# Optimization experiments

Measured on AMD Instinct MI355X. Metric: run time of the kernel, lower is better.

## Reference

```python
import jax, jax.numpy as jnp
import numpy as np

N, E, F_IN, HID, HEADS, B, CLASSES = 50000, 800000, 128, 64, 4, 512, 2


def setup_inputs() -> dict:
    key = jax.random.key(0)
    ks = jax.random.split(key, 20)
    s = 0.05
    inp = {
        "x": jax.random.normal(ks[0], (N, F_IN), jnp.float32),
        "edge_index": jax.random.randint(ks[1], (2, E), 0, N, jnp.int32),
        "batch": jnp.sort(jax.random.randint(ks[2], (N,), 0, B, jnp.int32)),
        # GCN layers (3): layer0 F_IN->HID, layers 1,2 HID->HID
        "gcn_w0": jax.random.normal(ks[3], (F_IN, HID), jnp.float32) * s,
        "gcn_b0": jnp.zeros((HID,), jnp.float32),
        "gcn_w1": jax.random.normal(ks[4], (HID, HID), jnp.float32) * s,
        "gcn_b1": jnp.zeros((HID,), jnp.float32),
        "gcn_w2": jax.random.normal(ks[5], (HID, HID), jnp.float32) * s,
        "gcn_b2": jnp.zeros((HID,), jnp.float32),
        # GAT: W [HID, HEADS*HID], attention vectors [HEADS, HID], bias [HID] (concat=False)
        "gat_w": jax.random.normal(ks[6], (HID, HEADS * HID), jnp.float32) * s,
        "gat_att_src": jax.random.normal(ks[7], (HEADS, HID), jnp.float32) * s,
        "gat_att_dst": jax.random.normal(ks[8], (HEADS, HID), jnp.float32) * s,
        "gat_b": jnp.zeros((HID,), jnp.float32),
        # MLP head
        "lin1_w": jax.random.normal(ks[9], (HID, HID // 2), jnp.float32) * s,
        "lin1_b": jnp.zeros((HID // 2,), jnp.float32),
        "lin2_w": jax.random.normal(ks[10], (HID // 2, CLASSES), jnp.float32) * s,
        "lin2_b": jnp.zeros((CLASSES,), jnp.float32),
    }
    return inp


def _forward(x, edge_index, batch,
             gcn_w0, gcn_b0, gcn_w1, gcn_b1, gcn_w2, gcn_b2,
             gat_w, gat_att_src, gat_att_dst, gat_b,
             lin1_w, lin1_b, lin2_w, lin2_b):
    n = x.shape[0]
    loop = jnp.arange(n, dtype=edge_index.dtype)
    src = jnp.concatenate([edge_index[0], loop])  # [E+N] with self-loops
    dst = jnp.concatenate([edge_index[1], loop])

    # symmetric GCN normalization (self-loops included, deg >= 1)
    deg = jax.ops.segment_sum(jnp.ones_like(dst, dtype=x.dtype), dst, num_segments=n)
    dinv = jax.lax.rsqrt(jnp.maximum(deg, 1.0))
    norm = dinv[src] * dinv[dst]  # [E+N]

    for W, b in ((gcn_w0, gcn_b0), (gcn_w1, gcn_b1), (gcn_w2, gcn_b2)):
        h = x @ W  # [N, HID]
        x = jax.ops.segment_sum(h[src] * norm[:, None], dst, num_segments=n) + b
        x = jax.nn.relu(x)  # dropout is identity in eval mode

    # GAT layer (heads=HEADS, concat=False -> mean over heads)
    H, C = gat_att_src.shape
    h = (x @ gat_w).reshape(n, H, C)  # [N, H, C]
    a_src = jnp.einsum('nhc,hc->nh', h, gat_att_src)
    a_dst = jnp.einsum('nhc,hc->nh', h, gat_att_dst)
    e = jax.nn.leaky_relu(a_src[src] + a_dst[dst], 0.2)  # [E+N, H]
    m = jax.ops.segment_max(e, dst, num_segments=n)      # per-dst softmax max
    p = jnp.exp(e - m[dst])
    denom = jax.ops.segment_sum(p, dst, num_segments=n)
    alpha = p / denom[dst]                                # [E+N, H]
    out = jax.ops.segment_sum(h[src] * alpha[:, :, None], dst, num_segments=n)
    x = jax.nn.relu(out.mean(axis=1) + gat_b)             # [N, HID]

    # global mean pool + global max pool over graphs
    cnt = jax.ops.segment_sum(jnp.ones((n,), x.dtype), batch, num_segments=B)
    mean_p = jax.ops.segment_sum(x, batch, num_segments=B) / jnp.maximum(cnt, 1.0)[:, None]
    max_p = jax.ops.segment_max(x, batch, num_segments=B)
    max_p = jnp.where(cnt[:, None] > 0, max_p, 0.0)
    g = mean_p + max_p  # [B, HID]

    g = jax.nn.relu(g @ lin1_w + lin1_b)
    return g @ lin2_w + lin2_b  # [B, CLASSES]


def reference(x, edge_index, batch,
              gcn_w0, gcn_b0, gcn_w1, gcn_b1, gcn_w2, gcn_b2,
              gat_w, gat_att_src, gat_att_dst, gat_b,
              lin1_w, lin1_b, lin2_w, lin2_b):
    return _forward(x, edge_index, batch,
                    gcn_w0, gcn_b0, gcn_w1, gcn_b1, gcn_w2, gcn_b2,
                    gat_w, gat_att_src, gat_att_dst, gat_b,
                    lin1_w, lin1_b, lin2_w, lin2_b)
```

## Files before the change

### kernel.cpp

```cpp
#include <hip/hip_runtime.h>
#include <math.h>

typedef short bf8 __attribute__((ext_vector_type(8)));
typedef _Float16 h8 __attribute__((ext_vector_type(8)));
typedef float f4 __attribute__((ext_vector_type(4)));
typedef unsigned short ushort_t;

#define BRANGE 128
#define NB_E 256

__device__ __forceinline__ int ilanebcast(int v, int l) {
  return __builtin_amdgcn_readlane(v, l);
}

__device__ __forceinline__ float wave_sum(float v) {
#pragma unroll
  for (int off = 32; off > 0; off >>= 1) v += __shfl_xor(v, off, 64);
  return v;
}

__device__ __forceinline__ ushort_t f2bf(float x) {
  unsigned int u = __float_as_uint(x);
  return (ushort_t)((u + 0x7fffu + ((u >> 16) & 1u)) >> 16);
}
__device__ __forceinline__ float b2f(ushort_t h) {
  return __uint_as_float(((unsigned int)h) << 16);
}

__global__ __launch_bounds__(256) void k_ehist(const int* __restrict__ dst,
                                               int* __restrict__ bhistT, int E, int nbuk) {
  __shared__ int h[512];
  int b = blockIdx.x, tid = threadIdx.x;
  for (int i = tid; i < nbuk; i += 256) h[i] = 0;
  __syncthreads();
  int chunk = (E + gridDim.x - 1) / gridDim.x;
  int e0 = b * chunk, e1 = min(E, e0 + chunk);
  for (int e = e0 + tid; e < e1; e += 256) atomicAdd(&h[dst[e] >> 7], 1);
  __syncthreads();
  for (int i = tid; i < nbuk; i += 256) bhistT[i * NB_E + b] = h[i];
}

__global__ __launch_bounds__(256) void k_btot(const int* __restrict__ bhistT,
                                              int* __restrict__ bcnt, int nb) {
  __shared__ int sm[256];
  int b = blockIdx.x, tid = threadIdx.x;
  sm[tid] = (tid < nb) ? bhistT[b * NB_E + tid] : 0;
  __syncthreads();
  for (int off = 128; off > 0; off >>= 1) {
    if (tid < off) sm[tid] += sm[tid + off];
    __syncthreads();
  }
  if (tid == 0) bcnt[b] = sm[0];
}

__global__ __launch_bounds__(512) void k_bscan(
    const int* __restrict__ bcnt, int* __restrict__ edgebase, int nbuk,
    int* __restrict__ rowstart, int n, int E) {
  __shared__ int smem[512];
  int t = threadIdx.x;
  int v = (t < nbuk) ? bcnt[t] : 0;
  smem[t] = v;
  __syncthreads();
  for (int off = 1; off < 512; off <<= 1) {
    int u = (t >= off) ? smem[t - off] : 0;
    __syncthreads();
    smem[t] += u;
    __syncthreads();
  }
  if (t < nbuk) edgebase[t] = smem[t] - v;
  if (t == 0) rowstart[n] = E + n;
}

__global__ __launch_bounds__(256) void k_bbase(int* __restrict__ bhistT,
                                               const int* __restrict__ edgebase,
                                               int nb) {
  __shared__ int sm[256];
  int b = blockIdx.x, tid = threadIdx.x;
  int v = (tid < nb) ? bhistT[b * NB_E + tid] : 0;
  sm[tid] = v;
  __syncthreads();
  for (int off = 1; off < 256; off <<= 1) {
    int u = (tid >= off) ? sm[tid - off] : 0;
    __syncthreads();
    sm[tid] += u;
    __syncthreads();
  }
  if (tid < nb) bhistT[b * NB_E + tid] = edgebase[b] + sm[tid] - v;
}

__global__ __launch_bounds__(256) void k_ebucket(
    const int* __restrict__ es, const int* __restrict__ ed,
    const int* __restrict__ bhistT, int* __restrict__ bedges, int E, int nbuk) {
  __shared__ int cur[512];
  int b = blockIdx.x, tid = threadIdx.x;
  for (int i = tid; i < nbuk; i += 256) cur[i] = bhistT[i * NB_E + b];
  __syncthreads();
  int chunk = (E + gridDim.x - 1) / gridDim.x;
  int e0 = b * chunk, e1 = min(E, e0 + chunk);
  for (int e = e0 + tid; e < e1; e += 256) {
    int s = es[e], d = ed[e];
    int pos = atomicAdd(&cur[d >> 7], 1);
    bedges[pos] = (s << 7) | (d & 127);
  }
}

__global__ __launch_bounds__(256) void k_ebsort(
    const int* __restrict__ bedges, const int* __restrict__ edgebase,
    const int* __restrict__ bcnt, int* __restrict__ colidx,
    int* __restrict__ rowstart, float* __restrict__ dinv, int n) {
  __shared__ int h[128];
  __shared__ int c[128];
  int b = blockIdx.x, tid = threadIdx.x;
  int nodes0 = b * BRANGE;
  int nnode = min(BRANGE, n - nodes0);
  int ebase = edgebase[b], ecnt = bcnt[b];
  int colbase = ebase + nodes0;
  if (tid < 128) h[tid] = (tid < nnode) ? 1 : 0;
  __syncthreads();
  for (int k = ebase + tid; k < ebase + ecnt; k += 256)
    atomicAdd(&h[bedges[k] & 127], 1);
  __syncthreads();
  int own = (tid < 128) ? h[tid] : 0;
  for (int off = 1; off < 128; off <<= 1) {
    int t = (tid >= off && tid < 128) ? h[tid - off] : 0;
    __syncthreads();
    if (tid < 128) h[tid] += t;
    __syncthreads();
  }
  if (tid < nnode) {
    int excl = h[tid] - own;
    int node = nodes0 + tid;
    rowstart[node] = colbase + excl;
    dinv[node] = 1.0f / sqrtf((float)own);
    colidx[colbase + excl] = node;
    c[tid] = excl + 1;
  }
  __syncthreads();
  for (int k = ebase + tid; k < ebase + ecnt; k += 256) {
    int p = bedges[k];
    int pos = atomicAdd(&c[p & 127], 1);
    colidx[colbase + pos] = p >> 7;
  }
}


__global__ void k_wswz0(const float* __restrict__ W, ushort_t* __restrict__ Bh,
                        ushort_t* __restrict__ Bl) {
  int e = blockIdx.x * 256 + threadIdx.x;
  if (e >= 4 * 4 * 64) return;
  int lane = e & 63, kc = (e >> 6) & 3, ct = e >> 8;
  int k0 = kc * 32 + (lane >> 4) * 8;
  int col = ct * 16 + (lane & 15);
#pragma unroll
  for (int j = 0; j < 8; j++) {
    float w = W[(k0 + j) * 64 + col];
    ushort_t h = f2bf(w);
    Bh[(size_t)e * 8 + j] = h;
    Bl[(size_t)e * 8 + j] = f2bf(w - b2f(h));
  }
}

__global__ void k_wswz1(const float* __restrict__ W, _Float16* __restrict__ Bh,
                        _Float16* __restrict__ Bl) {
  int e = blockIdx.x * 256 + threadIdx.x;
  if (e >= 8 * 64) return;
  int lane = e & 63, kc = (e >> 6) & 1, ct = e >> 7;
  int k0 = kc * 32 + (lane >> 4) * 8;
  int col = ct * 16 + (lane & 15);
#pragma unroll
  for (int j = 0; j < 8; j++) {
    float w = W[(k0 + j) * 64 + col];
    _Float16 h = (_Float16)w;
    Bh[(size_t)e * 8 + j] = h;
    Bl[(size_t)e * 8 + j] = (_Float16)(w - (float)h);
  }
}

__global__ void k_wswzg(const float* __restrict__ W, _Float16* __restrict__ Bh,
                        _Float16* __restrict__ Bl) {
  int e = blockIdx.x * 256 + threadIdx.x;
  if (e >= 4 * 8 * 64) return;
  int lane = e & 63, kc = (e >> 6) & 7, ct = e >> 9;
  int k0 = kc * 32 + (lane >> 4) * 8;
  int col = ct * 16 + (lane & 15);
#pragma unroll
  for (int j = 0; j < 8; j++) {
    int k = k0 + j;
    float w = W[(k & 63) * 256 + (k >> 6) * 64 + col];
    _Float16 h = (_Float16)w;
    Bh[(size_t)e * 8 + j] = h;
    Bl[(size_t)e * 8 + j] = (_Float16)(w - (float)h);
  }
}

__global__ void k_qpre(const float* __restrict__ W, const float* __restrict__ att_s,
                       const float* __restrict__ att_d,
                       float* __restrict__ q_src, float* __restrict__ q_dst) {
  int t = threadIdx.x;
  int h = t >> 6, k = t & 63;
  float ss = 0.0f, sd = 0.0f;
  for (int c = 0; c < 64; c++) {
    float w = W[k * 256 + h * 64 + c];
    ss = fmaf(w, att_s[h * 64 + c], ss);
    sd = fmaf(w, att_d[h * 64 + c], sd);
  }
  q_src[h * 64 + k] = ss;
  q_dst[h * 64 + k] = sd;
}

__global__ void k_qswz(const float* __restrict__ q_src, const float* __restrict__ q_dst,
                       _Float16* __restrict__ Bq) {
  int e = threadIdx.x;
  if (e >= 128) return;
  int lane = e & 63, kc = e >> 6;
  int k0 = kc * 32 + (lane >> 4) * 8;
  int col = lane & 15;
#pragma unroll
  for (int j = 0; j < 8; j++) {
    int k = k0 + j;
    float v = (col < 4) ? q_src[col * 64 + k]
                        : ((col < 8) ? q_dst[(col - 4) * 64 + k] : 0.0f);
    Bq[(size_t)e * 8 + j] = (_Float16)v;
  }
}

__global__ __launch_bounds__(256) void k_gemm0_mfma(
    const float* __restrict__ X, const ushort_t* __restrict__ Bh,
    const ushort_t* __restrict__ Bl, const float* __restrict__ dinv,
    _Float16* __restrict__ H, int n, int ntiles) {
  int tid = threadIdx.x, lane = tid & 63, wave = tid >> 6;
  int m = lane & 15, q = lane >> 4;
  for (int tile = blockIdx.x * 4 + wave; tile < ntiles; tile += gridDim.x * 4) {
    int ra = tile * 16 + m;
    if (ra >= n) ra = n - 1;
    const float* xrow = X + (size_t)ra * 128;
    f4 acc[4];
#pragma unroll
    for (int ct = 0; ct < 4; ct++) acc[ct] = (f4){0.f, 0.f, 0.f, 0.f};
#pragma unroll 2
    for (int kc = 0; kc < 4; kc++) {
      int ko = kc * 32 + q * 8;
      float4 xa = *(const float4*)(xrow + ko);
      float4 xb = *(const float4*)(xrow + ko + 4);
      float f[8] = {xa.x, xa.y, xa.z, xa.w, xb.x, xb.y, xb.z, xb.w};
      union { ushort_t u[8]; bf8 v; } Uh, Ul;
#pragma unroll
      for (int j = 0; j < 8; j++) {
        ushort_t h = f2bf(f[j]);
        Uh.u[j] = h;
        Ul.u[j] = f2bf(f[j] - b2f(h));
      }
#pragma unroll
      for (int ct = 0; ct < 4; ct++) {
        size_t boff = ((size_t)(ct * 4 + kc) * 64 + lane) * 8;
        bf8 bh = *(const bf8*)(Bh + boff);
        bf8 bl = *(const bf8*)(Bl + boff);
        acc[ct] = __builtin_amdgcn_mfma_f32_16x16x32_bf16(Uh.v, bh, acc[ct], 0, 0, 0);
        acc[ct] = __builtin_amdgcn_mfma_f32_16x16x32_bf16(Ul.v, bh, acc[ct], 0, 0, 0);
        acc[ct] = __builtin_amdgcn_mfma_f32_16x16x32_bf16(Uh.v, bl, acc[ct], 0, 0, 0);
      }
    }
#pragma unroll
    for (int r = 0; r < 4; r++) {
      int row = tile * 16 + q * 4 + r;
      if (row < n) {
        float dv = dinv[row];
#pragma unroll
        for (int ct = 0; ct < 4; ct++)
          H[(size_t)row * 64 + ct * 16 + m] = (_Float16)(acc[ct][r] * dv);
      }
    }
  }
}

__device__ __forceinline__ float gather_sum(const _Float16* __restrict__ h_in,
                                            const int* __restrict__ colidx,
                                            int s0, int s1, int lane) {
  float acc = 0.0f, accB = 0.0f;
  for (int base = s0; base < s1; base += 64) {
    int cnt = min(64, s1 - base);
    int myidx = (lane < cnt) ? colidx[base + lane] : 0;
    int k = 0;
    for (; k + 3 < cnt; k += 4) {
      int sa = ilanebcast(myidx, k);
      int sb = ilanebcast(myidx, k + 1);
      int sc = ilanebcast(myidx, k + 2);
      int sd = ilanebcast(myidx, k + 3);
      float va = (float)h_in[((size_t)sa << 6) + lane];
      float vb = (float)h_in[((size_t)sb << 6) + lane];
      float vc = (float)h_in[((size_t)sc << 6) + lane];
      float vd = (float)h_in[((size_t)sd << 6) + lane];
      acc += va; accB += vb; acc += vc; accB += vd;
    }
    for (; k < cnt; k++) {
      int sa = ilanebcast(myidx, k);
      acc += (float)h_in[((size_t)sa << 6) + lane];
    }
  }
  return acc + accB;
}

__global__ __launch_bounds__(1024) void k_agg_gemm_mfma(
    const _Float16* __restrict__ h_in, const float* __restrict__ dinv,
    const int* __restrict__ rowstart, const int* __restrict__ colidx,
    const float* __restrict__ bias, const _Float16* __restrict__ Bh,
    const _Float16* __restrict__ Bl, _Float16* __restrict__ h_out, int n) {
  __shared__ __align__(16) _Float16 xstage[16][72];
  int tid = threadIdx.x, lane = tid & 63, w = tid >> 6;
  int tile = blockIdx.x;
  int node = tile * 16 + w;
  float xv = 0.0f;
  if (node < n) {
    int s0 = rowstart[node], s1 = rowstart[node + 1];
    float a = gather_sum(h_in, colidx, s0, s1, lane);
    xv = fmaxf(fmaf(dinv[node], a, bias[lane]), 0.0f);
  }
  xstage[w][lane] = (_Float16)xv;
  __syncthreads();
  if (w < 4) {
    int m = lane & 15, q = lane >> 4, ct = w;
    h8 af0 = *(const h8*)&xstage[m][q * 8];
    h8 af1 = *(const h8*)&xstage[m][32 + q * 8];
    size_t o0 = ((size_t)(ct * 2 + 0) * 64 + lane) * 8;
    size_t o1 = ((size_t)(ct * 2 + 1) * 64 + lane) * 8;
    h8 bh0 = *(const h8*)(Bh + o0);
    h8 bh1 = *(const h8*)(Bh + o1);
    h8 bl0 = *(const h8*)(Bl + o0);
    h8 bl1 = *(const h8*)(Bl + o1);
    f4 acc = (f4){0.f, 0.f, 0.f, 0.f};
    acc = __builtin_amdgcn_mfma_f32_16x16x32_f16(af0, bh0, acc, 0, 0, 0);
    acc = __builtin_amdgcn_mfma_f32_16x16x32_f16(af1, bh1, acc, 0, 0, 0);
    acc = __builtin_amdgcn_mfma_f32_16x16x32_f16(af0, bl0, acc, 0, 0, 0);
    acc = __builtin_amdgcn_mfma_f32_16x16x32_f16(af1, bl1, acc, 0, 0, 0);
#pragma unroll
    for (int r = 0; r < 4; r++) {
      int n2 = tile * 16 + q * 4 + r;
      if (n2 < n)
        h_out[(size_t)n2 * 64 + ct * 16 + m] = (_Float16)(acc[r] * dinv[n2]);
    }
  }
}

__global__ __launch_bounds__(1024) void k_agg_gatpre_mfma(
    const _Float16* __restrict__ h_in, const float* __restrict__ dinv,
    const int* __restrict__ rowstart, const int* __restrict__ colidx,
    const float* __restrict__ bias, const _Float16* __restrict__ Bq,
    _Float16* __restrict__ x3, float* __restrict__ a_src, float* __restrict__ a_dst,
    int n) {
  __shared__ __align__(16) _Float16 xstage[16][72];
  int tid = threadIdx.x, lane = tid & 63, w = tid >> 6;
  int tile = blockIdx.x;
  int node = tile * 16 + w;
  float xv = 0.0f;
  if (node < n) {
    int s0 = rowstart[node], s1 = rowstart[node + 1];
    float a = gather_sum(h_in, colidx, s0, s1, lane);
    xv = fmaxf(fmaf(dinv[node], a, bias[lane]), 0.0f);
    x3[((size_t)node << 6) + lane] = (_Float16)xv;
  }
  xstage[w][lane] = (_Float16)xv;
  __syncthreads();
  if (w == 0) {
    int m = lane & 15, q = lane >> 4;
    h8 af0 = *(const h8*)&xstage[m][q * 8];
    h8 af1 = *(const h8*)&xstage[m][32 + q * 8];
    h8 bq0 = *(const h8*)(Bq + (size_t)lane * 8);
    h8 bq1 = *(const h8*)(Bq + (size_t)(64 + lane) * 8);
    f4 accL = (f4){0.f, 0.f, 0.f, 0.f};
    accL = __builtin_amdgcn_mfma_f32_16x16x32_f16(af0, bq0, accL, 0, 0, 0);
    accL = __builtin_amdgcn_mfma_f32_16x16x32_f16(af1, bq1, accL, 0, 0, 0);
#pragma unroll
    for (int r = 0; r < 4; r++) {
      int n2 = tile * 16 + q * 4 + r;
      if (n2 < n) {
        if (m < 4) a_src[(size_t)n2 * 4 + m] = accL[r];
        else if (m < 8) a_dst[(size_t)n2 * 4 + (m - 4)] = accL[r];
      }
    }
  }
}

__global__ __launch_bounds__(1024) void k_gat_fused(
    const _Float16* __restrict__ x3, const float* __restrict__ a_src,
    const float* __restrict__ a_dst, const int* __restrict__ rowstart,
    const int* __restrict__ colidx, const _Float16* __restrict__ Bh,
    const _Float16* __restrict__ Bl, const float* __restrict__ bias,
    float* __restrict__ out, int n) {
  __shared__ __align__(16) float4 wlds[16][64];
  __shared__ float astage[16][261];
  int tid = threadIdx.x, lane = tid & 63, w = tid >> 6;
  int tile = blockIdx.x;
  int node = tile * 16 + w;
  float v0 = 0.f, v1 = 0.f, v2 = 0.f, v3 = 0.f;
  if (node < n) {
    const float4 adv = *(const float4*)&a_dst[(size_t)node * 4];
    int s0 = rowstart[node], s1 = rowstart[node + 1];
    float acc0 = 0, acc1 = 0, acc2 = 0, acc3 = 0;
    float S0 = 0, S1 = 0, S2 = 0, S3 = 0;
    for (int base = s0; base < s1; base += 64) {
      int cnt = min(64, s1 - base);
      bool act = (lane < cnt);
      int myidx = act ? colidx[base + lane] : 0;
      float w0 = 0, w1 = 0, w2 = 0, w3 = 0;
      if (act) {
        const float4 as = *(const float4*)&a_src[(size_t)myidx * 4];
        float e0 = as.x + adv.x; e0 = (e0 > 0.f) ? e0 : 0.2f * e0; w0 = __expf(e0);
        float e1 = as.y + adv.y; e1 = (e1 > 0.f) ? e1 : 0.2f * e1; w1 = __expf(e1);
        float e2 = as.z + adv.z; e2 = (e2 > 0.f) ? e2 : 0.2f * e2; w2 = __expf(e2);
        float e3 = as.w + adv.w; e3 = (e3 > 0.f) ? e3 : 0.2f * e3; w3 = __expf(e3);
      }
      S0 += wave_sum(w0); S1 += wave_sum(w1);
      S2 += wave_sum(w2); S3 += wave_sum(w3);
      wlds[w][lane] = make_float4(w0, w1, w2, w3);
      int k = 0;
      for (; k + 3 < cnt; k += 4) {
        int sa = ilanebcast(myidx, k);
        int sb = ilanebcast(myidx, k + 1);
        int sc = ilanebcast(myidx, k + 2);
        int sd = ilanebcast(myidx, k + 3);
        float4 wa = wlds[w][k];
        float4 wb = wlds[w][k + 1];
        float4 wc = wlds[w][k + 2];
        float4 wd = wlds[w][k + 3];
        float va = (float)x3[((size_t)sa << 6) + lane];
        float vb = (float)x3[((size_t)sb << 6) + lane];
        float vc = (float)x3[((size_t)sc << 6) + lane];
        float vd = (float)x3[((size_t)sd << 6) + lane];
        acc0 = fmaf(wa.x, va, acc0); acc1 = fmaf(wa.y, va, acc1);
        acc2 = fmaf(wa.z, va, acc2); acc3 = fmaf(wa.w, va, acc3);
        acc0 = fmaf(wb.x, vb, acc0); acc1 = fmaf(wb.y, vb, acc1);
        acc2 = fmaf(wb.z, vb, acc2); acc3 = fmaf(wb.w, vb, acc3);
        acc0 = fmaf(wc.x, vc, acc0); acc1 = fmaf(wc.y, vc, acc1);
        acc2 = fmaf(wc.z, vc, acc2); acc3 = fmaf(wc.w, vc, acc3);
        acc0 = fmaf(wd.x, vd, acc0); acc1 = fmaf(wd.y, vd, acc1);
        acc2 = fmaf(wd.z, vd, acc2); acc3 = fmaf(wd.w, vd, acc3);
      }
      for (; k < cnt; k++) {
        int sa = ilanebcast(myidx, k);
        float4 wa = wlds[w][k];
        float va = (float)x3[((size_t)sa << 6) + lane];
        acc0 = fmaf(wa.x, va, acc0); acc1 = fmaf(wa.y, va, acc1);
        acc2 = fmaf(wa.z, va, acc2); acc3 = fmaf(wa.w, va, acc3);
      }
    }
    v0 = acc0 * (0.25f / S0);
    v1 = acc1 * (0.25f / S1);
    v2 = acc2 * (0.25f / S2);
    v3 = acc3 * (0.25f / S3);
  }
  astage[w][lane] = v0;
  astage[w][64 + lane] = v1;
  astage[w][128 + lane] = v2;
  astage[w][192 + lane] = v3;
  __syncthreads();
  if (w < 4) {
    int m = lane & 15, q = lane >> 4, ct = w;
    float bv = bias[ct * 16 + m];
    f4 acc = (f4){0.f, 0.f, 0.f, 0.f};
#pragma unroll 2
    for (int kc = 0; kc < 8; kc++) {
      const float* ap = &astage[m][kc * 32 + q * 8];
      union { _Float16 u[8]; h8 v; } Uh, Ul;
#pragma unroll
      for (int j = 0; j < 8; j++) {
        float a = ap[j];
        _Float16 h = (_Float16)a;
        Uh.u[j] = h;
        Ul.u[j] = (_Float16)(a - (float)h);
      }
      size_t boff = ((size_t)(ct * 8 + kc) * 64 + lane) * 8;
      h8 bh = *(const h8*)(Bh + boff);
      h8 bl = *(const h8*)(Bl + boff);
      acc = __builtin_amdgcn_mfma_f32_16x16x32_f16(Uh.v, bh, acc, 0, 0, 0);
      acc = __builtin_amdgcn_mfma_f32_16x16x32_f16(Ul.v, bh, acc, 0, 0, 0);
      acc = __builtin_amdgcn_mfma_f32_16x16x32_f16(Uh.v, bl, acc, 0, 0, 0);
    }
#pragma unroll
    for (int r = 0; r < 4; r++) {
      int row = tile * 16 + q * 4 + r;
      if (row < n)
        out[(size_t)row * 64 + ct * 16 + m] = fmaxf(acc[r] + bv, 0.f);
    }
  }
}

__global__ void k_gstart(const int* __restrict__ batch, int* gs, int n, int B) {
  int g = blockIdx.x * blockDim.x + threadIdx.x;
  if (g > B) return;
  int lo = 0, hi = n;
  while (lo < hi) {
    int mid = (lo + hi) >> 1;
    if (batch[mid] < g) lo = mid + 1; else hi = mid;
  }
  gs[g] = lo;
}

__global__ __launch_bounds__(256) void k_pool(const float* __restrict__ x,
                                              const int* __restrict__ gs,
                                              float* __restrict__ gvec, int B) {
  int g = (blockIdx.x * blockDim.x + threadIdx.x) >> 6;
  int lane = threadIdx.x & 63;
  if (g >= B) return;
  int s0 = gs[g], s1 = gs[g + 1];
  float sum = 0.0f, mx = -INFINITY;
  for (int nd = s0; nd < s1; ++nd) {
    float v = x[(size_t)nd * 64 + lane];
    sum += v;
    mx = fmaxf(mx, v);
  }
  int cnt = s1 - s0;
  float mean = sum / fmaxf((float)cnt, 1.0f);
  float mp = (cnt > 0) ? mx : 0.0f;
  gvec[g * 64 + lane] = mean + mp;
}

__global__ __launch_bounds__(256) void k_mlp(const float* __restrict__ gvec,
                                             const float* __restrict__ w1,
                                             const float* __restrict__ b1,
                                             const float* __restrict__ w2,
                                             const float* __restrict__ b2,
                                             float* __restrict__ out, int B) {
  int g = blockIdx.x * blockDim.x + threadIdx.x;
  if (g >= B) return;
  float gv[64];
#pragma unroll
  for (int i = 0; i < 64; i++) gv[i] = gvec[g * 64 + i];
  float o0 = b2[0], o1 = b2[1];
  for (int j = 0; j < 32; j++) {
    float a = b1[j];
#pragma unroll
    for (int i = 0; i < 64; i++) a = fmaf(gv[i], w1[i * 32 + j], a);
    a = fmaxf(a, 0.0f);
    o0 = fmaf(a, w2[j * 2 + 0], o0);
    o1 = fmaf(a, w2[j * 2 + 1], o1);
  }
  out[g * 2 + 0] = o0;
  out[g * 2 + 1] = o1;
}

extern "C" void kernel_launch(void* const* d_in, const int* in_sizes, int n_in,
                              void* d_out, int out_size, void* d_ws, size_t ws_size,
                              hipStream_t stream) {
  const float* x     = (const float*)d_in[0];
  const int*   ei    = (const int*)d_in[1];
  const int*   batch = (const int*)d_in[2];
  const float* w0 = (const float*)d_in[3];  const float* b0 = (const float*)d_in[4];
  const float* w1 = (const float*)d_in[5];  const float* b1 = (const float*)d_in[6];
  const float* w2 = (const float*)d_in[7];  const float* b2 = (const float*)d_in[8];
  const float* gat_w = (const float*)d_in[9];
  const float* att_s = (const float*)d_in[10];
  const float* att_d = (const float*)d_in[11];
  const float* gat_b = (const float*)d_in[12];
  const float* l1w = (const float*)d_in[13]; const float* l1b = (const float*)d_in[14];
  const float* l2w = (const float*)d_in[15]; const float* l2b = (const float*)d_in[16];

  const int N = in_sizes[0] / 128;
  const int E = in_sizes[1] / 2;
  const int B = out_size / 2;
  const int NT = (N + 15) / 16;
  const int NBUK = (N + BRANGE - 1) / BRANGE;

  char* ws = (char*)d_ws;
  size_t off = 0;
  auto alloc = [&](size_t bytes) -> void* {
    void* p = ws + off;
    off = (off + bytes + 255) & ~(size_t)255;
    return p;
  };
  int*       bhistT   = (int*)alloc((size_t)NBUK * NB_E * 4);
  int*       edgebase = (int*)alloc((size_t)NBUK * 4);
  int*       bcnt     = (int*)alloc((size_t)NBUK * 4);
  int*       bedges   = (int*)alloc((size_t)E * 4);
  int*       rowstart = (int*)alloc((size_t)(N + 1) * 4);
  int*       colidx   = (int*)alloc((size_t)(E + N) * 4);
  float*     dinv     = (float*)alloc((size_t)N * 4);
  _Float16*  hbuf     = (_Float16*)alloc((size_t)N * 64 * 2);
  _Float16*  hbuf2    = (_Float16*)alloc((size_t)N * 64 * 2);
  _Float16*  xg       = (_Float16*)alloc((size_t)N * 64 * 2);
  float*     gatout   = (float*)alloc((size_t)N * 64 * 4);
  float*     a_src    = (float*)alloc((size_t)N * 4 * 4);
  float*     a_dst    = (float*)alloc((size_t)N * 4 * 4);
  float*     q_src    = (float*)alloc(4 * 64 * 4);
  float*     q_dst    = (float*)alloc(4 * 64 * 4);
  ushort_t*  B0h      = (ushort_t*)alloc(4 * 4 * 64 * 8 * 2);
  ushort_t*  B0l      = (ushort_t*)alloc(4 * 4 * 64 * 8 * 2);
  _Float16*  Bw1h     = (_Float16*)alloc(8 * 64 * 8 * 2);
  _Float16*  Bw1l     = (_Float16*)alloc(8 * 64 * 8 * 2);
  _Float16*  Bw2h     = (_Float16*)alloc(8 * 64 * 8 * 2);
  _Float16*  Bw2l     = (_Float16*)alloc(8 * 64 * 8 * 2);
  _Float16*  Bq       = (_Float16*)alloc(2 * 64 * 8 * 2);
  _Float16*  Bgh      = (_Float16*)alloc(4 * 8 * 64 * 8 * 2);
  _Float16*  Bgl      = (_Float16*)alloc(4 * 8 * 64 * 8 * 2);
  int*       gs       = (int*)alloc((size_t)(B + 1) * 4);
  float*     gvec     = (float*)alloc((size_t)B * 64 * 4);
  (void)ws_size; (void)n_in;

  k_ehist<<<NB_E, 256, 0, stream>>>(ei + E, bhistT, E, NBUK);
  k_btot<<<NBUK, 256, 0, stream>>>(bhistT, bcnt, NB_E);
  k_bscan<<<1, 512, 0, stream>>>(bcnt, edgebase, NBUK, rowstart, N, E);
  k_bbase<<<NBUK, 256, 0, stream>>>(bhistT, edgebase, NB_E);
  k_ebucket<<<NB_E, 256, 0, stream>>>(ei, ei + E, bhistT, bedges, E, NBUK);
  k_ebsort<<<NBUK, 256, 0, stream>>>(bedges, edgebase, bcnt, colidx, rowstart, dinv, N);
  k_qpre<<<1, 256, 0, stream>>>(gat_w, att_s, att_d, q_src, q_dst);
  k_qswz<<<1, 256, 0, stream>>>(q_src, q_dst, Bq);
  k_wswz0<<<4, 256, 0, stream>>>(w0, B0h, B0l);
  k_wswz1<<<2, 256, 0, stream>>>(w1, Bw1h, Bw1l);
  k_wswz1<<<2, 256, 0, stream>>>(w2, Bw2h, Bw2l);
  k_wswzg<<<8, 256, 0, stream>>>(gat_w, Bgh, Bgl);

  k_gemm0_mfma<<<1024, 256, 0, stream>>>(x, B0h, B0l, dinv, hbuf, N, NT);
  k_agg_gemm_mfma<<<NT, 1024, 0, stream>>>(hbuf, dinv, rowstart, colidx, b0,
                                           Bw1h, Bw1l, hbuf2, N);
  k_agg_gemm_mfma<<<NT, 1024, 0, stream>>>(hbuf2, dinv, rowstart, colidx, b1,
                                           Bw2h, Bw2l, hbuf, N);
  k_agg_gatpre_mfma<<<NT, 1024, 0, stream>>>(hbuf, dinv, rowstart, colidx, b2,
                                             Bq, xg, a_src, a_dst, N);
  k_gat_fused<<<NT, 1024, 0, stream>>>(xg, a_src, a_dst, rowstart, colidx,
                                       Bgh, Bgl, gat_b, gatout, N);
  k_gstart<<<(B + 1 + 255) / 256, 256, 0, stream>>>(batch, gs, N, B);
  k_pool<<<(B + 3) / 4, 256, 0, stream>>>(gatout, gs, gvec, B);
  k_mlp<<<(B + 255) / 256, 256, 0, stream>>>(gvec, l1w, l1b, l2w, l2b, (float*)d_out, B);
}
```

Before: 374.2 us.

## Merge setup and tail kernels, deepen gather unroll, use 32-bit gather indexing

Collapses the four weight-swizzle kernels into one launch, fuses the q precompute with its swizzle through shared memory, and merges the graph-start search, pooling and MLP into a single kernel. This cuts the kernel launch count and the intermediate global buffers. The GCN gather loop now processes 8 neighbors per step instead of 4, and gather addresses use 32-bit int math instead of size_t. The goal is to lower launch overhead and raise memory-level parallelism in the aggregation kernels, at the cost of more registers. The 32-bit indexing stays within range for N*64.

```diff
diff --git a/kernel.cpp b/kernel.cpp
--- a/kernel.cpp
+++ b/kernel.cpp
@@ -143,59 +143,59 @@
   }
 }
 
-
-__global__ void k_wswz0(const float* __restrict__ W, ushort_t* __restrict__ Bh,
-                        ushort_t* __restrict__ Bl) {
-  int e = blockIdx.x * 256 + threadIdx.x;
-  if (e >= 4 * 4 * 64) return;
-  int lane = e & 63, kc = (e >> 6) & 3, ct = e >> 8;
-  int k0 = kc * 32 + (lane >> 4) * 8;
-  int col = ct * 16 + (lane & 15);
-#pragma unroll
-  for (int j = 0; j < 8; j++) {
-    float w = W[(k0 + j) * 64 + col];
-    ushort_t h = f2bf(w);
-    Bh[(size_t)e * 8 + j] = h;
-    Bl[(size_t)e * 8 + j] = f2bf(w - b2f(h));
-  }
-}
-
-__global__ void k_wswz1(const float* __restrict__ W, _Float16* __restrict__ Bh,
-                        _Float16* __restrict__ Bl) {
-  int e = blockIdx.x * 256 + threadIdx.x;
-  if (e >= 8 * 64) return;
-  int lane = e & 63, kc = (e >> 6) & 1, ct = e >> 7;
-  int k0 = kc * 32 + (lane >> 4) * 8;
-  int col = ct * 16 + (lane & 15);
-#pragma unroll
-  for (int j = 0; j < 8; j++) {
-    float w = W[(k0 + j) * 64 + col];
-    _Float16 h = (_Float16)w;
-    Bh[(size_t)e * 8 + j] = h;
-    Bl[(size_t)e * 8 + j] = (_Float16)(w - (float)h);
-  }
-}
-
-__global__ void k_wswzg(const float* __restrict__ W, _Float16* __restrict__ Bh,
-                        _Float16* __restrict__ Bl) {
-  int e = blockIdx.x * 256 + threadIdx.x;
-  if (e >= 4 * 8 * 64) return;
-  int lane = e & 63, kc = (e >> 6) & 7, ct = e >> 9;
-  int k0 = kc * 32 + (lane >> 4) * 8;
-  int col = ct * 16 + (lane & 15);
-#pragma unroll
-  for (int j = 0; j < 8; j++) {
-    int k = k0 + j;
-    float w = W[(k & 63) * 256 + (k >> 6) * 64 + col];
-    _Float16 h = (_Float16)w;
-    Bh[(size_t)e * 8 + j] = h;
-    Bl[(size_t)e * 8 + j] = (_Float16)(w - (float)h);
-  }
-}
-
-__global__ void k_qpre(const float* __restrict__ W, const float* __restrict__ att_s,
-                       const float* __restrict__ att_d,
-                       float* __restrict__ q_src, float* __restrict__ q_dst) {
+__global__ __launch_bounds__(256) void k_wswz_all(
+    const float* __restrict__ W0, ushort_t* __restrict__ B0h, ushort_t* __restrict__ B0l,
+    const float* __restrict__ W1, _Float16* __restrict__ Bw1h, _Float16* __restrict__ Bw1l,
+    const float* __restrict__ W2, _Float16* __restrict__ Bw2h, _Float16* __restrict__ Bw2l,
+    const float* __restrict__ Wg, _Float16* __restrict__ Bgh, _Float16* __restrict__ Bgl) {
+  int bid = blockIdx.x, tid = threadIdx.x;
+  if (bid < 4) {
+    int e = bid * 256 + tid;
+    int lane = e & 63, kc = (e >> 6) & 3, ct = e >> 8;
+    int k0 = kc * 32 + (lane >> 4) * 8;
+    int col = ct * 16 + (lane & 15);
+#pragma unroll
+    for (int j = 0; j < 8; j++) {
+      float w = W0[(k0 + j) * 64 + col];
+      ushort_t h = f2bf(w);
+      B0h[(size_t)e * 8 + j] = h;
+      B0l[(size_t)e * 8 + j] = f2bf(w - b2f(h));
+    }
+  } else if (bid < 8) {
+    const float* W = (bid < 6) ? W1 : W2;
+    _Float16* Bh = (bid < 6) ? Bw1h : Bw2h;
+    _Float16* Bl = (bid < 6) ? Bw1l : Bw2l;
+    int e = ((bid - 4) & 1) * 256 + tid;
+    int lane = e & 63, kc = (e >> 6) & 1, ct = e >> 7;
+    int k0 = kc * 32 + (lane >> 4) * 8;
+    int col = ct * 16 + (lane & 15);
+#pragma unroll
+    for (int j = 0; j < 8; j++) {
+      float w = W[(k0 + j) * 64 + col];
+      _Float16 h = (_Float16)w;
+      Bh[(size_t)e * 8 + j] = h;
+      Bl[(size_t)e * 8 + j] = (_Float16)(w - (float)h);
+    }
+  } else {
+    int e = (bid - 8) * 256 + tid;
+    int lane = e & 63, kc = (e >> 6) & 7, ct = e >> 9;
+    int k0 = kc * 32 + (lane >> 4) * 8;
+    int col = ct * 16 + (lane & 15);
+#pragma unroll
+    for (int j = 0; j < 8; j++) {
+      int k = k0 + j;
+      float w = Wg[(k & 63) * 256 + (k >> 6) * 64 + col];
+      _Float16 h = (_Float16)w;
+      Bgh[(size_t)e * 8 + j] = h;
+      Bgl[(size_t)e * 8 + j] = (_Float16)(w - (float)h);
+    }
+  }
+}
+
+__global__ __launch_bounds__(256) void k_qprep(
+    const float* __restrict__ W, const float* __restrict__ att_s,
+    const float* __restrict__ att_d, _Float16* __restrict__ Bq) {
+  __shared__ float qs[256], qd[256];
   int t = threadIdx.x;
   int h = t >> 6, k = t & 63;
   float ss = 0.0f, sd = 0.0f;
@@ -204,23 +204,20 @@
     ss = fmaf(w, att_s[h * 64 + c], ss);
     sd = fmaf(w, att_d[h * 64 + c], sd);
   }
-  q_src[h * 64 + k] = ss;
-  q_dst[h * 64 + k] = sd;
-}
-
-__global__ void k_qswz(const float* __restrict__ q_src, const float* __restrict__ q_dst,
-                       _Float16* __restrict__ Bq) {
-  int e = threadIdx.x;
-  if (e >= 128) return;
-  int lane = e & 63, kc = e >> 6;
-  int k0 = kc * 32 + (lane >> 4) * 8;
-  int col = lane & 15;
-#pragma unroll
-  for (int j = 0; j < 8; j++) {
-    int k = k0 + j;
-    float v = (col < 4) ? q_src[col * 64 + k]
-                        : ((col < 8) ? q_dst[(col - 4) * 64 + k] : 0.0f);
-    Bq[(size_t)e * 8 + j] = (_Float16)v;
+  qs[h * 64 + k] = ss;
+  qd[h * 64 + k] = sd;
+  __syncthreads();
+  if (t < 128) {
+    int lane = t & 63, kc = t >> 6;
+    int k0 = kc * 32 + (lane >> 4) * 8;
+    int col = lane & 15;
+#pragma unroll
+    for (int j = 0; j < 8; j++) {
+      int kk = k0 + j;
+      float v = (col < 4) ? qs[col * 64 + kk]
+                          : ((col < 8) ? qd[(col - 4) * 64 + kk] : 0.0f);
+      Bq[(size_t)t * 8 + j] = (_Float16)v;
+    }
   }
 }
 
@@ -281,20 +278,37 @@
     int cnt = min(64, s1 - base);
     int myidx = (lane < cnt) ? colidx[base + lane] : 0;
     int k = 0;
+    for (; k + 7 < cnt; k += 8) {
+      int i0 = (ilanebcast(myidx, k) << 6) + lane;
+      int i1 = (ilanebcast(myidx, k + 1) << 6) + lane;
+      int i2 = (ilanebcast(myidx, k + 2) << 6) + lane;
+      int i3 = (ilanebcast(myidx, k + 3) << 6) + lane;
+      int i4 = (ilanebcast(myidx, k + 4) << 6) + lane;
+      int i5 = (ilanebcast(myidx, k + 5) << 6) + lane;
+      int i6 = (ilanebcast(myidx, k + 6) << 6) + lane;
+      int i7 = (ilanebcast(myidx, k + 7) << 6) + lane;
+      float v0 = (float)h_in[i0];
+      float v1 = (float)h_in[i1];
+      float v2 = (float)h_in[i2];
+      float v3 = (float)h_in[i3];
+      float v4 = (float)h_in[i4];
+      float v5 = (float)h_in[i5];
+      float v6 = (float)h_in[i6];
+      float v7 = (float)h_in[i7];
+      acc += v0; accB += v1; acc += v2; accB += v3;
+      acc += v4; accB += v5; acc += v6; accB += v7;
+    }
     for (; k + 3 < cnt; k += 4) {
-      int sa = ilanebcast(myidx, k);
-      int sb = ilanebcast(myidx, k + 1);
-      int sc = ilanebcast(myidx, k + 2);
-      int sd = ilanebcast(myidx, k + 3);
-      float va = (float)h_in[((size_t)sa << 6) + lane];
-      float vb = (float)h_in[((size_t)sb << 6) + lane];
-      float vc = (float)h_in[((size_t)sc << 6) + lane];
-      float vd = (float)h_in[((size_t)sd << 6) + lane];
-      acc += va; accB += vb; acc += vc; accB += vd;
+      int i0 = (ilanebcast(myidx, k) << 6) + lane;
+      int i1 = (ilanebcast(myidx, k + 1) << 6) + lane;
+      int i2 = (ilanebcast(myidx, k + 2) << 6) + lane;
+      int i3 = (ilanebcast(myidx, k + 3) << 6) + lane;
+      acc += (float)h_in[i0]; accB += (float)h_in[i1];
+      acc += (float)h_in[i2]; accB += (float)h_in[i3];
     }
     for (; k < cnt; k++) {
-      int sa = ilanebcast(myidx, k);
-      acc += (float)h_in[((size_t)sa << 6) + lane];
+      int i0 = (ilanebcast(myidx, k) << 6) + lane;
+      acc += (float)h_in[i0];
     }
   }
   return acc + accB;
@@ -356,7 +370,7 @@
     int s0 = rowstart[node], s1 = rowstart[node + 1];
     float a = gather_sum(h_in, colidx, s0, s1, lane);
     xv = fmaxf(fmaf(dinv[node], a, bias[lane]), 0.0f);
-    x3[((size_t)node << 6) + lane] = (_Float16)xv;
+    x3[(node << 6) + lane] = (_Float16)xv;
   }
   xstage[w][lane] = (_Float16)xv;
   __syncthreads();
@@ -414,18 +428,18 @@
       wlds[w][lane] = make_float4(w0, w1, w2, w3);
       int k = 0;
       for (; k + 3 < cnt; k += 4) {
-        int sa = ilanebcast(myidx, k);
-        int sb = ilanebcast(myidx, k + 1);
-        int sc = ilanebcast(myidx, k + 2);
-        int sd = ilanebcast(myidx, k + 3);
+        int i0 = (ilanebcast(myidx, k) << 6) + lane;
+        int i1 = (ilanebcast(myidx, k + 1) << 6) + lane;
+        int i2 = (ilanebcast(myidx, k + 2) << 6) + lane;
+        int i3 = (ilanebcast(myidx, k + 3) << 6) + lane;
         float4 wa = wlds[w][k];
         float4 wb = wlds[w][k + 1];
         float4 wc = wlds[w][k + 2];
         float4 wd = wlds[w][k + 3];
-        float va = (float)x3[((size_t)sa << 6) + lane];
-        float vb = (float)x3[((size_t)sb << 6) + lane];
-        float vc = (float)x3[((size_t)sc << 6) + lane];
-        float vd = (float)x3[((size_t)sd << 6) + lane];
+        float va = (float)x3[i0];
+        float vb = (float)x3[i1];
+        float vc = (float)x3[i2];
+        float vd = (float)x3[i3];
         acc0 = fmaf(wa.x, va, acc0); acc1 = fmaf(wa.y, va, acc1);
         acc2 = fmaf(wa.z, va, acc2); acc3 = fmaf(wa.w, va, acc3);
         acc0 = fmaf(wb.x, vb, acc0); acc1 = fmaf(wb.y, vb, acc1);
@@ -436,9 +450,9 @@
         acc2 = fmaf(wd.z, vd, acc2); acc3 = fmaf(wd.w, vd, acc3);
       }
       for (; k < cnt; k++) {
-        int sa = ilanebcast(myidx, k);
+        int i0 = (ilanebcast(myidx, k) << 6) + lane;
         float4 wa = wlds[w][k];
-        float va = (float)x3[((size_t)sa << 6) + lane];
+        float va = (float)x3[i0];
         acc0 = fmaf(wa.x, va, acc0); acc1 = fmaf(wa.y, va, acc1);
         acc2 = fmaf(wa.z, va, acc2); acc3 = fmaf(wa.w, va, acc3);
       }
@@ -484,24 +498,21 @@
   }
 }
 
-__global__ void k_gstart(const int* __restrict__ batch, int* gs, int n, int B) {
-  int g = blockIdx.x * blockDim.x + threadIdx.x;
-  if (g > B) return;
+__global__ __launch_bounds__(256) void k_pool_mlp(
+    const float* __restrict__ x, const int* __restrict__ batch,
+    const float* __restrict__ w1, const float* __restrict__ b1,
+    const float* __restrict__ w2, const float* __restrict__ b2,
+    float* __restrict__ out, int n, int B) {
+  __shared__ float gls[4][64];
+  int tid = threadIdx.x, lane = tid & 63, w = tid >> 6;
+  int g = blockIdx.x * 4 + w;
+  if (g >= B) return;
   int lo = 0, hi = n;
-  while (lo < hi) {
-    int mid = (lo + hi) >> 1;
-    if (batch[mid] < g) lo = mid + 1; else hi = mid;
-  }
-  gs[g] = lo;
-}
-
-__global__ __launch_bounds__(256) void k_pool(const float* __restrict__ x,
-                                              const int* __restrict__ gs,
-                                              float* __restrict__ gvec, int B) {
-  int g = (blockIdx.x * blockDim.x + threadIdx.x) >> 6;
-  int lane = threadIdx.x & 63;
-  if (g >= B) return;
-  int s0 = gs[g], s1 = gs[g + 1];
+  while (lo < hi) { int mid = (lo + hi) >> 1; if (batch[mid] < g) lo = mid + 1; else hi = mid; }
+  int s0 = lo;
+  lo = 0; hi = n;
+  while (lo < hi) { int mid = (lo + hi) >> 1; if (batch[mid] < g + 1) lo = mid + 1; else hi = mid; }
+  int s1 = lo;
   float sum = 0.0f, mx = -INFINITY;
   for (int nd = s0; nd < s1; ++nd) {
     float v = x[(size_t)nd * 64 + lane];
@@ -511,31 +522,21 @@
   int cnt = s1 - s0;
   float mean = sum / fmaxf((float)cnt, 1.0f);
   float mp = (cnt > 0) ? mx : 0.0f;
-  gvec[g * 64 + lane] = mean + mp;
-}
-
-__global__ __launch_bounds__(256) void k_mlp(const float* __restrict__ gvec,
-                                             const float* __restrict__ w1,
-                                             const float* __restrict__ b1,
-                                             const float* __restrict__ w2,
-                                             const float* __restrict__ b2,
-                                             float* __restrict__ out, int B) {
-  int g = blockIdx.x * blockDim.x + threadIdx.x;
-  if (g >= B) return;
-  float gv[64];
-#pragma unroll
-  for (int i = 0; i < 64; i++) gv[i] = gvec[g * 64 + i];
-  float o0 = b2[0], o1 = b2[1];
-  for (int j = 0; j < 32; j++) {
-    float a = b1[j];
-#pragma unroll
-    for (int i = 0; i < 64; i++) a = fmaf(gv[i], w1[i * 32 + j], a);
+  gls[w][lane] = mean + mp;
+  float a = 0.0f;
+  if (lane < 32) {
+    a = b1[lane];
+    for (int i = 0; i < 64; i++) a = fmaf(gls[w][i], w1[i * 32 + lane], a);
     a = fmaxf(a, 0.0f);
-    o0 = fmaf(a, w2[j * 2 + 0], o0);
-    o1 = fmaf(a, w2[j * 2 + 1], o1);
-  }
-  out[g * 2 + 0] = o0;
-  out[g * 2 + 1] = o1;
+  }
+  float p0 = (lane < 32) ? a * w2[lane * 2 + 0] : 0.0f;
+  float p1 = (lane < 32) ? a * w2[lane * 2 + 1] : 0.0f;
+  p0 = wave_sum(p0);
+  p1 = wave_sum(p1);
+  if (lane == 0) {
+    out[g * 2 + 0] = b2[0] + p0;
+    out[g * 2 + 1] = b2[1] + p1;
+  }
 }
 
 extern "C" void kernel_launch(void* const* d_in, const int* in_sizes, int n_in,
@@ -580,8 +581,6 @@
   float*     gatout   = (float*)alloc((size_t)N * 64 * 4);
   float*     a_src    = (float*)alloc((size_t)N * 4 * 4);
   float*     a_dst    = (float*)alloc((size_t)N * 4 * 4);
-  float*     q_src    = (float*)alloc(4 * 64 * 4);
-  float*     q_dst    = (float*)alloc(4 * 64 * 4);
   ushort_t*  B0h      = (ushort_t*)alloc(4 * 4 * 64 * 8 * 2);
   ushort_t*  B0l      = (ushort_t*)alloc(4 * 4 * 64 * 8 * 2);
   _Float16*  Bw1h     = (_Float16*)alloc(8 * 64 * 8 * 2);
@@ -591,8 +590,6 @@
   _Float16*  Bq       = (_Float16*)alloc(2 * 64 * 8 * 2);
   _Float16*  Bgh      = (_Float16*)alloc(4 * 8 * 64 * 8 * 2);
   _Float16*  Bgl      = (_Float16*)alloc(4 * 8 * 64 * 8 * 2);
-  int*       gs       = (int*)alloc((size_t)(B + 1) * 4);
-  float*     gvec     = (float*)alloc((size_t)B * 64 * 4);
   (void)ws_size; (void)n_in;
 
   k_ehist<<<NB_E, 256, 0, stream>>>(ei + E, bhistT, E, NBUK);
@@ -601,12 +598,9 @@
   k_bbase<<<NBUK, 256, 0, stream>>>(bhistT, edgebase, NB_E);
   k_ebucket<<<NB_E, 256, 0, stream>>>(ei, ei + E, bhistT, bedges, E, NBUK);
   k_ebsort<<<NBUK, 256, 0, stream>>>(bedges, edgebase, bcnt, colidx, rowstart, dinv, N);
-  k_qpre<<<1, 256, 0, stream>>>(gat_w, att_s, att_d, q_src, q_dst);
-  k_qswz<<<1, 256, 0, stream>>>(q_src, q_dst, Bq);
-  k_wswz0<<<4, 256, 0, stream>>>(w0, B0h, B0l);
-  k_wswz1<<<2, 256, 0, stream>>>(w1, Bw1h, Bw1l);
-  k_wswz1<<<2, 256, 0, stream>>>(w2, Bw2h, Bw2l);
-  k_wswzg<<<8, 256, 0, stream>>>(gat_w, Bgh, Bgl);
+  k_qprep<<<1, 256, 0, stream>>>(gat_w, att_s, att_d, Bq);
+  k_wswz_all<<<16, 256, 0, stream>>>(w0, B0h, B0l, w1, Bw1h, Bw1l,
+                                     w2, Bw2h, Bw2l, gat_w, Bgh, Bgl);
 
   k_gemm0_mfma<<<1024, 256, 0, stream>>>(x, B0h, B0l, dinv, hbuf, N, NT);
   k_agg_gemm_mfma<<<NT, 1024, 0, stream>>>(hbuf, dinv, rowstart, colidx, b0,
@@ -617,7 +611,6 @@
                                              Bq, xg, a_src, a_dst, N);
   k_gat_fused<<<NT, 1024, 0, stream>>>(xg, a_src, a_dst, rowstart, colidx,
                                        Bgh, Bgl, gat_b, gatout, N);
-  k_gstart<<<(B + 1 + 255) / 256, 256, 0, stream>>>(batch, gs, N, B);
-  k_pool<<<(B + 3) / 4, 256, 0, stream>>>(gatout, gs, gvec, B);
-  k_mlp<<<(B + 255) / 256, 256, 0, stream>>>(gvec, l1w, l1b, l2w, l2b, (float*)d_out, B);
-}
+  k_pool_mlp<<<(B + 3) / 4, 256, 0, stream>>>(gatout, batch, l1w, l1b, l2w, l2b,
+                                              (float*)d_out, N, B);
+}
```

Measured after the change: 342.3 us, median of 2. 1.09x faster.
